# Performance work log

Measured on AMD Instinct MI355X. Metric: run time of the kernel, lower is better.

## Reference

```python
import jax, jax.numpy as jnp
import numpy as np
from jax.ops import segment_sum

N_NODES = 100000


def _gcn_layer(x, W, b, src, dst, n_nodes):
    # DGL GraphConv with norm='both': out = D_in^{-1/2} A D_out^{-1/2} x W + b
    # degrees clamped to min 1 (DGL behavior, handles zero-degree nodes)
    ones_e = jnp.ones(src.shape[0], dtype=x.dtype)
    deg_out = jnp.clip(segment_sum(ones_e, src, num_segments=n_nodes), 1.0)
    deg_in = jnp.clip(segment_sum(ones_e, dst, num_segments=n_nodes), 1.0)
    h = x * jax.lax.rsqrt(deg_out)[:, None]            # [N, F] source norm
    agg = segment_sum(h[src], dst, num_segments=n_nodes)  # [N, F] sum over in-edges
    agg = agg * jax.lax.rsqrt(deg_in)[:, None]          # dest norm
    return agg @ W + b


def setup_inputs() -> dict:
    key = jax.random.key(0)
    k1, k2, k3, k4, k5 = jax.random.split(key, 5)
    E = 1600000
    x = jax.random.normal(k1, (N_NODES, 128), dtype=jnp.float32)
    edge_src = jax.random.randint(k2, (E,), 0, N_NODES, dtype=jnp.int32)
    edge_dst = jax.random.randint(k3, (E,), 0, N_NODES, dtype=jnp.int32)
    W1 = jax.random.normal(k4, (128, 64), dtype=jnp.float32) * (1.0 / np.sqrt(128))
    b1 = jnp.zeros((64,), dtype=jnp.float32)
    W2 = jax.random.normal(k5, (64, 64), dtype=jnp.float32) * (1.0 / np.sqrt(64))
    b2 = jnp.zeros((64,), dtype=jnp.float32)
    return {"x": x, "edge_src": edge_src, "edge_dst": edge_dst,
            "W1": W1, "b1": b1, "W2": W2, "b2": b2}


def reference(x, edge_src, edge_dst, W1, b1, W2, b2):
    h = _gcn_layer(x, W1, b1, edge_src, edge_dst, N_NODES)
    h = jax.nn.relu(h)
    out = _gcn_layer(h, W2, b2, edge_src, edge_dst, N_NODES)
    return out
```

## Files before the change

### kernel.cpp

```cpp
#include <hip/hip_runtime.h>
#include <hip/hip_fp16.h>


static inline size_t align256(size_t x) { return (x + 255) & ~(size_t)255; }

#define BKT_SHIFT 8
#define BKT_W 256
#define MAX_NBK 400
#define CAP 5120
#define SC_BLOCKS 256
#define SC_THREADS 512

typedef _Float16 f16x8 __attribute__((ext_vector_type(8)));
typedef float f32x4 __attribute__((ext_vector_type(4)));

__global__ __launch_bounds__(SC_THREADS)
void scatter_atomic_kernel(const int* __restrict__ src, const int* __restrict__ dst,
                           int* __restrict__ gcnt_d, int* __restrict__ gcnt_s,
                           int* __restrict__ ebuf, unsigned char* __restrict__ sbuf,
                           int nbk, int E, int slice_len) {
    __shared__ int hd[MAX_NBK];
    __shared__ int hs[MAX_NBK];
    __shared__ int cur_d[MAX_NBK];
    __shared__ int cur_s[MAX_NBK];
    const int b = blockIdx.x;
    const int t = threadIdx.x;
    for (int i = t; i < nbk; i += SC_THREADS) { hd[i] = 0; hs[i] = 0; }
    __syncthreads();
    const int beg = b * slice_len;
    const int end = min(beg + slice_len, E);
    for (int i = beg + t; i < end; i += SC_THREADS) {
        atomicAdd(&hd[dst[i] >> BKT_SHIFT], 1);
        atomicAdd(&hs[src[i] >> BKT_SHIFT], 1);
    }
    __syncthreads();
    for (int i = t; i < nbk; i += SC_THREADS) {
        int c = hd[i];
        cur_d[i] = i * CAP + (c ? atomicAdd(&gcnt_d[i], c) : 0);
        c = hs[i];
        cur_s[i] = i * CAP + (c ? atomicAdd(&gcnt_s[i], c) : 0);
    }
    __syncthreads();
    for (int i = beg + t; i < end; i += SC_THREADS) {
        int d = dst[i], s = src[i];
        int pd = atomicAdd(&cur_d[d >> BKT_SHIFT], 1);
        ebuf[pd] = ((d & (BKT_W - 1)) << 17) | s;
        int ps = atomicAdd(&cur_s[s >> BKT_SHIFT], 1);
        sbuf[ps] = (unsigned char)(s & (BKT_W - 1));
    }
}

__global__ __launch_bounds__(512)
void bucket_csr_kernel(const int* __restrict__ ebuf,
                       const unsigned char* __restrict__ sbuf,
                       const int* __restrict__ gcnt_d, const int* __restrict__ gcnt_s,
                       int* __restrict__ csr_src,
                       int* __restrict__ cnt_in, int* __restrict__ cnt_out,
                       int* __restrict__ row_ptr,
                       int nbk, int N, int E) {
    __shared__ int cnt[BKT_W];
    __shared__ int rp[BKT_W];
    __shared__ int cur[BKT_W];
    __shared__ int cnts[BKT_W];
    __shared__ int red[512];
    __shared__ int sh_db;
    const int k = blockIdx.x;
    const int lo = k << BKT_SHIFT;
    const int span = min(BKT_W, N - lo);
    const int t = threadIdx.x;

    int s1 = 0;
    for (int i = t; i < k; i += 512) s1 += gcnt_d[i];
    red[t] = s1;
    __syncthreads();
    for (int off = 256; off >= 1; off >>= 1) {
        if (t < off) red[t] += red[t + off];
        __syncthreads();
    }
    if (t == 0) sh_db = red[0];
    __syncthreads();
    const int db = sh_db;
    const int eb = k * CAP, ee = eb + gcnt_d[k];
    const int sb = k * CAP, se = sb + gcnt_s[k];

    if (t < BKT_W) { cnt[t] = 0; cnts[t] = 0; }
    __syncthreads();
    for (int i = eb + t; i < ee; i += 512) atomicAdd(&cnt[ebuf[i] >> 17], 1);
    for (int i = sb + t; i < se; i += 512) atomicAdd(&cnts[sbuf[i]], 1);
    __syncthreads();
    if (t < BKT_W) rp[t] = cnt[t];
    __syncthreads();
    for (int off = 1; off < BKT_W; off <<= 1) {
        int v = (t < BKT_W && t >= off) ? rp[t - off] : 0;
        __syncthreads();
        if (t < BKT_W) rp[t] += v;
        __syncthreads();
    }
    if (t < span) {
        row_ptr[lo + t] = db + rp[t] - cnt[t];
        cnt_in[lo + t]  = cnt[t];
        cnt_out[lo + t] = cnts[t];
    }
    __syncthreads();
    if (t < BKT_W) cur[t] = db + rp[t] - cnt[t];
    __syncthreads();
    for (int i = eb + t; i < ee; i += 512) {
        int p = ebuf[i];
        int pos = atomicAdd(&cur[p >> 17], 1);
        csr_src[pos] = p & 0x1FFFF;
    }
    if (k == 0 && t == 0) row_ptr[N] = E;
}

template <int K>
__global__ __launch_bounds__(256)
void gemm_scale_kernel(const float* __restrict__ X, const float* __restrict__ W,
                       const int* __restrict__ cnt_out,
                       __half* __restrict__ Y, int N) {
    __shared__ _Float16 Wt[2][64][K + 8];
    const int t = threadIdx.x;
    {
        const int jj = t >> 2;
        const int kb = (t & 3) * (K / 4);
#pragma unroll
        for (int c8 = 0; c8 < K / 4; c8 += 8) {
            float w[8];
#pragma unroll
            for (int m = 0; m < 8; ++m) w[m] = W[(kb + c8 + m) * 64 + jj];
            f16x8 hi8, lo8;
#pragma unroll
            for (int m = 0; m < 8; ++m) {
                const _Float16 h = (_Float16)w[m];
                hi8[m] = h;
                lo8[m] = (_Float16)(w[m] - (float)h);
            }
            *(f16x8*)&Wt[0][jj][kb + c8] = hi8;
            *(f16x8*)&Wt[1][jj][kb + c8] = lo8;
        }
    }
    __syncthreads();

    const int wid  = t >> 6;
    const int lane = t & 63;
    const int col  = lane & 15;
    const int kg   = (lane >> 4) * 8;

    const int rowA = blockIdx.x * 64 + wid * 16 + col;
    const size_t xbase = (size_t)min(rowA, N - 1) * K;

    f32x4 acc0 = {}, acc1 = {}, acc2 = {}, acc3 = {};

#pragma unroll
    for (int ks = 0; ks < K; ks += 32) {
        float4 xa = *(const float4*)&X[xbase + ks + kg];
        float4 xb = *(const float4*)&X[xbase + ks + kg + 4];
        const float xs[8] = {xa.x, xa.y, xa.z, xa.w, xb.x, xb.y, xb.z, xb.w};
        f16x8 ahi, alo;
#pragma unroll
        for (int j = 0; j < 8; ++j) {
            const _Float16 h = (_Float16)xs[j];
            ahi[j] = h;
            alo[j] = (_Float16)(xs[j] - (float)h);
        }
#pragma unroll
        for (int tile = 0; tile < 4; ++tile) {
            const f16x8 bhi = *(const f16x8*)&Wt[0][col + 16 * tile][ks + kg];
            const f16x8 blo = *(const f16x8*)&Wt[1][col + 16 * tile][ks + kg];
            f32x4* acc = (tile == 0) ? &acc0 : (tile == 1) ? &acc1
                       : (tile == 2) ? &acc2 : &acc3;
            *acc = __builtin_amdgcn_mfma_f32_16x16x32_f16(ahi, bhi, *acc, 0, 0, 0);
            *acc = __builtin_amdgcn_mfma_f32_16x16x32_f16(alo, bhi, *acc, 0, 0, 0);
            *acc = __builtin_amdgcn_mfma_f32_16x16x32_f16(ahi, blo, *acc, 0, 0, 0);
        }
    }

    const int rbase = blockIdx.x * 64 + wid * 16 + (lane >> 4) * 4;
#pragma unroll
    for (int r = 0; r < 4; ++r) {
        const int rr = rbase + r;
        if (rr < N) {
            const float sc = rsqrtf((float)max(cnt_out[rr], 1));
            __half* yp = &Y[(size_t)rr * 64 + col];
            yp[0]  = __float2half_rn(acc0[r] * sc);
            yp[16] = __float2half_rn(acc1[r] * sc);
            yp[32] = __float2half_rn(acc2[r] * sc);
            yp[48] = __float2half_rn(acc3[r] * sc);
        }
    }
}

__global__ __launch_bounds__(256)
void agg_gemm_kernel(const __half* __restrict__ Y,
                     const int* __restrict__ row_ptr,
                     const int* __restrict__ csr_src,
                     const int* __restrict__ cnt_in,
                     const int* __restrict__ cnt_out,
                     const float* __restrict__ b1,
                     const float* __restrict__ W2,
                     __half* __restrict__ Y2, int N) {
    __shared__ _Float16 Hh[32][72];
    __shared__ _Float16 Hl[32][72];
    const int t = threadIdx.x;
    const int wid  = t >> 6;
    const int lane = t & 63;
    const int col  = lane & 15;
    const int kg   = (lane >> 4) * 8;

    const int nl = t >> 3;
    const int f8 = t & 7;
    const int n  = blockIdx.x * 32 + nl;
    const int nc = min(n, N - 1);

    const int start = row_ptr[nc];
    const int end   = row_ptr[nc + 1];
    const int last  = end - 1;

    float4 acc0 = {0.f, 0.f, 0.f, 0.f}, acc1 = {0.f, 0.f, 0.f, 0.f};
    for (int e = start; e < end; e += 12) {
        int idx[12];
#pragma unroll
        for (int j = 0; j < 12; ++j) idx[j] = csr_src[min(e + j, last)];
        uint4 v[12];
#pragma unroll
        for (int j = 0; j < 12; ++j)
            v[j] = *((const uint4*)(Y + ((size_t)idx[j] << 6)) + f8);
#pragma unroll
        for (int j = 0; j < 12; ++j) {
            if (e + j < end) {
                float2 a = __half22float2(*(const __half2*)&v[j].x);
                float2 b = __half22float2(*(const __half2*)&v[j].y);
                float2 c = __half22float2(*(const __half2*)&v[j].z);
                float2 d = __half22float2(*(const __half2*)&v[j].w);
                acc0.x += a.x; acc0.y += a.y; acc0.z += b.x; acc0.w += b.y;
                acc1.x += c.x; acc1.y += c.y; acc1.z += d.x; acc1.w += d.y;
            }
        }
    }

    float wb[16];
#pragma unroll
    for (int m = 0; m < 8; ++m) {
        wb[m]     = W2[(kg + m) * 64 + 16 * wid + col];
        wb[m + 8] = W2[(32 + kg + m) * 64 + 16 * wid + col];
    }

    {
        const float sc = rsqrtf((float)max(cnt_in[nc], 1));
        const float4 bb0 = *(const float4*)&b1[8 * f8];
        const float4 bb1 = *(const float4*)&b1[8 * f8 + 4];
        float hv[8];
        hv[0] = fmaxf(acc0.x * sc + bb0.x, 0.f);
        hv[1] = fmaxf(acc0.y * sc + bb0.y, 0.f);
        hv[2] = fmaxf(acc0.z * sc + bb0.z, 0.f);
        hv[3] = fmaxf(acc0.w * sc + bb0.w, 0.f);
        hv[4] = fmaxf(acc1.x * sc + bb1.x, 0.f);
        hv[5] = fmaxf(acc1.y * sc + bb1.y, 0.f);
        hv[6] = fmaxf(acc1.z * sc + bb1.z, 0.f);
        hv[7] = fmaxf(acc1.w * sc + bb1.w, 0.f);
        f16x8 hh, hl;
#pragma unroll
        for (int q = 0; q < 8; ++q) {
            const _Float16 hi = (_Float16)hv[q];
            hh[q] = hi;
            hl[q] = (_Float16)(hv[q] - (float)hi);
        }
        *(f16x8*)&Hh[nl][8 * f8] = hh;
        *(f16x8*)&Hl[nl][8 * f8] = hl;
    }
    __syncthreads();

    f16x8 bhi0, blo0, bhi1, blo1;
#pragma unroll
    for (int m = 0; m < 8; ++m) {
        _Float16 h = (_Float16)wb[m];
        bhi0[m] = h;
        blo0[m] = (_Float16)(wb[m] - (float)h);
        h = (_Float16)wb[m + 8];
        bhi1[m] = h;
        blo1[m] = (_Float16)(wb[m + 8] - (float)h);
    }

    const int rloc = (lane >> 4) * 4;
#pragma unroll
    for (int g = 0; g < 2; ++g) {
        const f16x8 ahi0 = *(const f16x8*)&Hh[g * 16 + col][kg];
        const f16x8 alo0 = *(const f16x8*)&Hl[g * 16 + col][kg];
        const f16x8 ahi1 = *(const f16x8*)&Hh[g * 16 + col][32 + kg];
        const f16x8 alo1 = *(const f16x8*)&Hl[g * 16 + col][32 + kg];

        f32x4 acc2 = {};
        acc2 = __builtin_amdgcn_mfma_f32_16x16x32_f16(ahi0, bhi0, acc2, 0, 0, 0);
        acc2 = __builtin_amdgcn_mfma_f32_16x16x32_f16(alo0, bhi0, acc2, 0, 0, 0);
        acc2 = __builtin_amdgcn_mfma_f32_16x16x32_f16(ahi0, blo0, acc2, 0, 0, 0);
        acc2 = __builtin_amdgcn_mfma_f32_16x16x32_f16(ahi1, bhi1, acc2, 0, 0, 0);
        acc2 = __builtin_amdgcn_mfma_f32_16x16x32_f16(alo1, bhi1, acc2, 0, 0, 0);
        acc2 = __builtin_amdgcn_mfma_f32_16x16x32_f16(ahi1, blo1, acc2, 0, 0, 0);

#pragma unroll
        for (int r = 0; r < 4; ++r) {
            const int rr = blockIdx.x * 32 + g * 16 + rloc + r;
            if (rr < N) {
                const float s2 = rsqrtf((float)max(cnt_out[rr], 1));
                Y2[(size_t)rr * 64 + 16 * wid + col] = __float2half_rn(acc2[r] * s2);
            }
        }
    }
}

template <bool RELU>
__global__ __launch_bounds__(256)
void aggregate_kernel(const __half* __restrict__ Y,
                      const int* __restrict__ row_ptr,
                      const int* __restrict__ csr_src,
                      const int* __restrict__ cnt_in,
                      const float* __restrict__ bias,
                      float* __restrict__ out, int N) {
    const int n = blockIdx.x * 32 + (threadIdx.x >> 3);
    if (n >= N) return;
    const int f8 = threadIdx.x & 7;

    const int start = row_ptr[n];
    const int end   = row_ptr[n + 1];
    const int last  = end - 1;

    float4 acc0 = {0.f, 0.f, 0.f, 0.f}, acc1 = {0.f, 0.f, 0.f, 0.f};
    for (int e = start; e < end; e += 12) {
        int idx[12];
#pragma unroll
        for (int j = 0; j < 12; ++j) idx[j] = csr_src[min(e + j, last)];
        uint4 v[12];
#pragma unroll
        for (int j = 0; j < 12; ++j)
            v[j] = *((const uint4*)(Y + ((size_t)idx[j] << 6)) + f8);
#pragma unroll
        for (int j = 0; j < 12; ++j) {
            if (e + j < end) {
                float2 a = __half22float2(*(const __half2*)&v[j].x);
                float2 b = __half22float2(*(const __half2*)&v[j].y);
                float2 c = __half22float2(*(const __half2*)&v[j].z);
                float2 d = __half22float2(*(const __half2*)&v[j].w);
                acc0.x += a.x; acc0.y += a.y; acc0.z += b.x; acc0.w += b.y;
                acc1.x += c.x; acc1.y += c.y; acc1.z += d.x; acc1.w += d.y;
            }
        }
    }

    const float sc = rsqrtf((float)max(cnt_in[n], 1));
    const float4 bb0 = *(const float4*)&bias[8 * f8];
    const float4 bb1 = *(const float4*)&bias[8 * f8 + 4];
    float4 o0, o1;
    o0.x = acc0.x * sc + bb0.x;
    o0.y = acc0.y * sc + bb0.y;
    o0.z = acc0.z * sc + bb0.z;
    o0.w = acc0.w * sc + bb0.w;
    o1.x = acc1.x * sc + bb1.x;
    o1.y = acc1.y * sc + bb1.y;
    o1.z = acc1.z * sc + bb1.z;
    o1.w = acc1.w * sc + bb1.w;
    if (RELU) {
        o0.x = fmaxf(o0.x, 0.f); o0.y = fmaxf(o0.y, 0.f);
        o0.z = fmaxf(o0.z, 0.f); o0.w = fmaxf(o0.w, 0.f);
        o1.x = fmaxf(o1.x, 0.f); o1.y = fmaxf(o1.y, 0.f);
        o1.z = fmaxf(o1.z, 0.f); o1.w = fmaxf(o1.w, 0.f);
    }
    float4* op = (float4*)&out[((size_t)n << 6) + 8 * f8];
    op[0] = o0;
    op[1] = o1;
}

extern "C" void kernel_launch(void* const* d_in, const int* in_sizes, int n_in,
                              void* d_out, int out_size, void* d_ws, size_t ws_size,
                              hipStream_t stream) {
    const float* x   = (const float*)d_in[0];
    const int*   src = (const int*)d_in[1];
    const int*   dst = (const int*)d_in[2];
    const float* W1  = (const float*)d_in[3];
    const float* b1  = (const float*)d_in[4];
    const float* W2  = (const float*)d_in[5];
    const float* b2  = (const float*)d_in[6];
    float* out = (float*)d_out;

    const int N = in_sizes[0] / 128;
    const int E = in_sizes[1];

    const int nbk = (N + BKT_W - 1) >> BKT_SHIFT;

    char* ws = (char*)d_ws;
    size_t off = 0;
    __half* Y       = (__half*)(ws + off); off = align256(off + (size_t)N * 64 * sizeof(__half));
    __half* Y2      = (__half*)(ws + off); off = align256(off + (size_t)N * 64 * sizeof(__half));
    int* csr_src    = (int*)(ws + off);    off = align256(off + (size_t)E * sizeof(int));
    int* ebuf       = (int*)(ws + off);    off = align256(off + (size_t)nbk * CAP * sizeof(int));
    unsigned char* sbuf = (unsigned char*)(ws + off); off = align256(off + (size_t)nbk * CAP);
    int* gcnt       = (int*)(ws + off);    off = align256(off + (size_t)2 * nbk * sizeof(int));
    int* gcnt_d     = gcnt;
    int* gcnt_s     = gcnt + nbk;
    int* cnt_out    = (int*)(ws + off);    off = align256(off + (size_t)N * sizeof(int));
    int* cnt_in     = (int*)(ws + off);    off = align256(off + (size_t)N * sizeof(int));
    int* row_ptr    = (int*)(ws + off);    off = align256(off + (size_t)(N + 1) * sizeof(int));

    const int pslice = (E + SC_BLOCKS - 1) / SC_BLOCKS;

    hipMemsetAsync(gcnt, 0, (size_t)2 * nbk * sizeof(int), stream);
    scatter_atomic_kernel<<<SC_BLOCKS, SC_THREADS, 0, stream>>>(
        src, dst, gcnt_d, gcnt_s, ebuf, sbuf, nbk, E, pslice);
    bucket_csr_kernel<<<nbk, 512, 0, stream>>>(ebuf, sbuf, gcnt_d, gcnt_s, csr_src,
                                               cnt_in, cnt_out, row_ptr, nbk, N, E);

    const int gemm_blocks = (N + 63) / 64;
    const int agg_blocks  = (N + 31) / 32;

    gemm_scale_kernel<128><<<gemm_blocks, 256, 0, stream>>>(x, W1, cnt_out, Y, N);
    agg_gemm_kernel<<<agg_blocks, 256, 0, stream>>>(Y, row_ptr, csr_src,
                                                    cnt_in, cnt_out, b1, W2, Y2, N);
    aggregate_kernel<false><<<agg_blocks, 256, 0, stream>>>(Y2, row_ptr, csr_src,
                                                            cnt_in, b2, out, N);
}
```

Baseline: 237.1 us.

## Fuse graph bucket scatter and CSR build into one cooperative kernel

Replaces the memset, bucket scatter kernel and per-bucket CSR kernel with one cooperative kernel that zeroes the counters, builds per-block histograms and scatters edges. It then builds the per-bucket CSR, with grid-wide syncs between the phases. The aim is to remove two launch boundaries and the separate memset. The grid size is now set by occupancy (up to 512 blocks) and CSR buckets are spread across blocks with a grid-stride loop. The cost is the grid.sync barriers and a cooperative launch, which may carry its own overhead.

Measured after the change: 545.8 us. +130.2%, slower.

```diff
diff --git a/kernel.cpp b/kernel.cpp
--- a/kernel.cpp
+++ b/kernel.cpp
@@ -1,5 +1,8 @@
 #include <hip/hip_runtime.h>
 #include <hip/hip_fp16.h>
+#include <hip/hip_cooperative_groups.h>
+
+namespace cg = cooperative_groups;
 
 
 static inline size_t align256(size_t x) { return (x + 255) & ~(size_t)255; }
@@ -8,108 +11,110 @@
 #define BKT_W 256
 #define MAX_NBK 400
 #define CAP 5120
-#define SC_BLOCKS 256
-#define SC_THREADS 512
+#define BD_THREADS 512
+#define BD_MAX_BLOCKS 512
 
 typedef _Float16 f16x8 __attribute__((ext_vector_type(8)));
 typedef float f32x4 __attribute__((ext_vector_type(4)));
 
-__global__ __launch_bounds__(SC_THREADS)
-void scatter_atomic_kernel(const int* __restrict__ src, const int* __restrict__ dst,
-                           int* __restrict__ gcnt_d, int* __restrict__ gcnt_s,
-                           int* __restrict__ ebuf, unsigned char* __restrict__ sbuf,
-                           int nbk, int E, int slice_len) {
-    __shared__ int hd[MAX_NBK];
-    __shared__ int hs[MAX_NBK];
-    __shared__ int cur_d[MAX_NBK];
-    __shared__ int cur_s[MAX_NBK];
+__global__ __launch_bounds__(BD_THREADS)
+void build_kernel(const int* __restrict__ src, const int* __restrict__ dst,
+                  int* __restrict__ gcnt_d, int* __restrict__ gcnt_s,
+                  int* __restrict__ ebuf, unsigned char* __restrict__ sbuf,
+                  int* __restrict__ csr_src,
+                  int* __restrict__ cnt_in, int* __restrict__ cnt_out,
+                  int* __restrict__ row_ptr,
+                  int nbk, int N, int E)
+{
+    cg::grid_group grid = cg::this_grid();
+    const int t = threadIdx.x;
     const int b = blockIdx.x;
-    const int t = threadIdx.x;
-    for (int i = t; i < nbk; i += SC_THREADS) { hd[i] = 0; hs[i] = 0; }
+    const int nb = gridDim.x;
+
+    __shared__ union {
+        struct { int hd[MAX_NBK], hs[MAX_NBK], cd[MAX_NBK], cs[MAX_NBK]; } part;
+        struct { int cnt[BKT_W], rp[BKT_W], cur[BKT_W], cnts[BKT_W],
+                 red[BD_THREADS], db; } csr;
+    } u;
+
+    for (int i = b * BD_THREADS + t; i < 2 * nbk; i += nb * BD_THREADS)
+        gcnt_d[i] = 0;
+    for (int i = t; i < nbk; i += BD_THREADS) { u.part.hd[i] = 0; u.part.hs[i] = 0; }
     __syncthreads();
-    const int beg = b * slice_len;
-    const int end = min(beg + slice_len, E);
-    for (int i = beg + t; i < end; i += SC_THREADS) {
-        atomicAdd(&hd[dst[i] >> BKT_SHIFT], 1);
-        atomicAdd(&hs[src[i] >> BKT_SHIFT], 1);
+    const int slice = (E + nb - 1) / nb;
+    const int beg = b * slice;
+    const int iend = min(beg + slice, E);
+    for (int i = beg + t; i < iend; i += BD_THREADS) {
+        atomicAdd(&u.part.hd[dst[i] >> BKT_SHIFT], 1);
+        atomicAdd(&u.part.hs[src[i] >> BKT_SHIFT], 1);
     }
     __syncthreads();
-    for (int i = t; i < nbk; i += SC_THREADS) {
-        int c = hd[i];
-        cur_d[i] = i * CAP + (c ? atomicAdd(&gcnt_d[i], c) : 0);
-        c = hs[i];
-        cur_s[i] = i * CAP + (c ? atomicAdd(&gcnt_s[i], c) : 0);
+    __threadfence();
+    grid.sync();
+    for (int i = t; i < nbk; i += BD_THREADS) {
+        int c = u.part.hd[i];
+        u.part.cd[i] = i * CAP + (c ? atomicAdd(&gcnt_d[i], c) : 0);
+        c = u.part.hs[i];
+        u.part.cs[i] = i * CAP + (c ? atomicAdd(&gcnt_s[i], c) : 0);
     }
     __syncthreads();
-    for (int i = beg + t; i < end; i += SC_THREADS) {
+    for (int i = beg + t; i < iend; i += BD_THREADS) {
         int d = dst[i], s = src[i];
-        int pd = atomicAdd(&cur_d[d >> BKT_SHIFT], 1);
+        int pd = atomicAdd(&u.part.cd[d >> BKT_SHIFT], 1);
         ebuf[pd] = ((d & (BKT_W - 1)) << 17) | s;
-        int ps = atomicAdd(&cur_s[s >> BKT_SHIFT], 1);
+        int ps = atomicAdd(&u.part.cs[s >> BKT_SHIFT], 1);
         sbuf[ps] = (unsigned char)(s & (BKT_W - 1));
     }
-}
-
-__global__ __launch_bounds__(512)
-void bucket_csr_kernel(const int* __restrict__ ebuf,
-                       const unsigned char* __restrict__ sbuf,
-                       const int* __restrict__ gcnt_d, const int* __restrict__ gcnt_s,
-                       int* __restrict__ csr_src,
-                       int* __restrict__ cnt_in, int* __restrict__ cnt_out,
-                       int* __restrict__ row_ptr,
-                       int nbk, int N, int E) {
-    __shared__ int cnt[BKT_W];
-    __shared__ int rp[BKT_W];
-    __shared__ int cur[BKT_W];
-    __shared__ int cnts[BKT_W];
-    __shared__ int red[512];
-    __shared__ int sh_db;
-    const int k = blockIdx.x;
-    const int lo = k << BKT_SHIFT;
-    const int span = min(BKT_W, N - lo);
-    const int t = threadIdx.x;
-
-    int s1 = 0;
-    for (int i = t; i < k; i += 512) s1 += gcnt_d[i];
-    red[t] = s1;
-    __syncthreads();
-    for (int off = 256; off >= 1; off >>= 1) {
-        if (t < off) red[t] += red[t + off];
-        __syncthreads();
-    }
-    if (t == 0) sh_db = red[0];
-    __syncthreads();
-    const int db = sh_db;
-    const int eb = k * CAP, ee = eb + gcnt_d[k];
-    const int sb = k * CAP, se = sb + gcnt_s[k];
-
-    if (t < BKT_W) { cnt[t] = 0; cnts[t] = 0; }
-    __syncthreads();
-    for (int i = eb + t; i < ee; i += 512) atomicAdd(&cnt[ebuf[i] >> 17], 1);
-    for (int i = sb + t; i < se; i += 512) atomicAdd(&cnts[sbuf[i]], 1);
-    __syncthreads();
-    if (t < BKT_W) rp[t] = cnt[t];
-    __syncthreads();
-    for (int off = 1; off < BKT_W; off <<= 1) {
-        int v = (t < BKT_W && t >= off) ? rp[t - off] : 0;
-        __syncthreads();
-        if (t < BKT_W) rp[t] += v;
-        __syncthreads();
-    }
-    if (t < span) {
-        row_ptr[lo + t] = db + rp[t] - cnt[t];
-        cnt_in[lo + t]  = cnt[t];
-        cnt_out[lo + t] = cnts[t];
-    }
-    __syncthreads();
-    if (t < BKT_W) cur[t] = db + rp[t] - cnt[t];
-    __syncthreads();
-    for (int i = eb + t; i < ee; i += 512) {
-        int p = ebuf[i];
-        int pos = atomicAdd(&cur[p >> 17], 1);
-        csr_src[pos] = p & 0x1FFFF;
-    }
-    if (k == 0 && t == 0) row_ptr[N] = E;
+    __threadfence();
+    grid.sync();
+
+    for (int k = b; k < nbk; k += nb) {
+        const int lo = k << BKT_SHIFT;
+        const int span = min(BKT_W, N - lo);
+
+        int s1 = 0;
+        for (int i = t; i < k; i += BD_THREADS) s1 += gcnt_d[i];
+        u.csr.red[t] = s1;
+        __syncthreads();
+        for (int off = BD_THREADS / 2; off >= 1; off >>= 1) {
+            if (t < off) u.csr.red[t] += u.csr.red[t + off];
+            __syncthreads();
+        }
+        if (t == 0) u.csr.db = u.csr.red[0];
+        __syncthreads();
+        const int db = u.csr.db;
+        const int eb = k * CAP, ee = eb + gcnt_d[k];
+        const int sb = k * CAP, se = sb + gcnt_s[k];
+
+        if (t < BKT_W) { u.csr.cnt[t] = 0; u.csr.cnts[t] = 0; }
+        __syncthreads();
+        for (int i = eb + t; i < ee; i += BD_THREADS) atomicAdd(&u.csr.cnt[ebuf[i] >> 17], 1);
+        for (int i = sb + t; i < se; i += BD_THREADS) atomicAdd(&u.csr.cnts[sbuf[i]], 1);
+        __syncthreads();
+        if (t < BKT_W) u.csr.rp[t] = u.csr.cnt[t];
+        __syncthreads();
+        for (int off = 1; off < BKT_W; off <<= 1) {
+            int v = (t < BKT_W && t >= off) ? u.csr.rp[t - off] : 0;
+            __syncthreads();
+            if (t < BKT_W) u.csr.rp[t] += v;
+            __syncthreads();
+        }
+        if (t < span) {
+            row_ptr[lo + t] = db + u.csr.rp[t] - u.csr.cnt[t];
+            cnt_in[lo + t]  = u.csr.cnt[t];
+            cnt_out[lo + t] = u.csr.cnts[t];
+        }
+        __syncthreads();
+        if (t < BKT_W) u.csr.cur[t] = db + u.csr.rp[t] - u.csr.cnt[t];
+        __syncthreads();
+        for (int i = eb + t; i < ee; i += BD_THREADS) {
+            int p = ebuf[i];
+            int pos = atomicAdd(&u.csr.cur[p >> 17], 1);
+            csr_src[pos] = p & 0x1FFFF;
+        }
+        if (k == 0 && t == 0) row_ptr[N] = E;
+        __syncthreads();
+    }
 }
 
 template <int K>
@@ -371,19 +376,18 @@
 extern "C" void kernel_launch(void* const* d_in, const int* in_sizes, int n_in,
                               void* d_out, int out_size, void* d_ws, size_t ws_size,
                               hipStream_t stream) {
-    const float* x   = (const float*)d_in[0];
     const int*   src = (const int*)d_in[1];
     const int*   dst = (const int*)d_in[2];
+    const float* x   = (const float*)d_in[0];
     const float* W1  = (const float*)d_in[3];
     const float* b1  = (const float*)d_in[4];
     const float* W2  = (const float*)d_in[5];
     const float* b2  = (const float*)d_in[6];
     float* out = (float*)d_out;
 
-    const int N = in_sizes[0] / 128;
-    const int E = in_sizes[1];
-
-    const int nbk = (N + BKT_W - 1) >> BKT_SHIFT;
+    int N = in_sizes[0] / 128;
+    int E = in_sizes[1];
+    int nbk = (N + BKT_W - 1) >> BKT_SHIFT;
 
     char* ws = (char*)d_ws;
     size_t off = 0;
@@ -399,13 +403,21 @@
     int* cnt_in     = (int*)(ws + off);    off = align256(off + (size_t)N * sizeof(int));
     int* row_ptr    = (int*)(ws + off);    off = align256(off + (size_t)(N + 1) * sizeof(int));
 
-    const int pslice = (E + SC_BLOCKS - 1) / SC_BLOCKS;
-
-    hipMemsetAsync(gcnt, 0, (size_t)2 * nbk * sizeof(int), stream);
-    scatter_atomic_kernel<<<SC_BLOCKS, SC_THREADS, 0, stream>>>(
-        src, dst, gcnt_d, gcnt_s, ebuf, sbuf, nbk, E, pslice);
-    bucket_csr_kernel<<<nbk, 512, 0, stream>>>(ebuf, sbuf, gcnt_d, gcnt_s, csr_src,
-                                               cnt_in, cnt_out, row_ptr, nbk, N, E);
+    static int s_blocks = -1;
+    if (s_blocks < 0) {
+        hipDeviceProp_t prop;
+        hipGetDeviceProperties(&prop, 0);
+        int nb = 0;
+        hipOccupancyMaxActiveBlocksPerMultiprocessor(&nb, build_kernel, BD_THREADS, 0);
+        if (nb < 1) nb = 1;
+        long cap = (long)nb * prop.multiProcessorCount;
+        s_blocks = (int)((cap < BD_MAX_BLOCKS) ? cap : BD_MAX_BLOCKS);
+    }
+
+    void* args[] = {&src, &dst, &gcnt_d, &gcnt_s, &ebuf, &sbuf,
+                    &csr_src, &cnt_in, &cnt_out, &row_ptr, &nbk, &N, &E};
+    hipLaunchCooperativeKernel((const void*)build_kernel, dim3(s_blocks),
+                               dim3(BD_THREADS), args, 0, stream);
 
     const int gemm_blocks = (N + 63) / 64;
     const int agg_blocks  = (N + 31) / 32;
```
